# Performance work log

Measured on AMD Instinct MI355X. Metric: run time of the kernel, lower is better.

## Reference

```python
import jax, jax.numpy as jnp
import numpy as np

N = 50000   # num nodes
E = 800000  # num edges
D = 128     # in_features
C = 1.0     # curvature c
MIN_NORM = 1e-15
BALL_EPS = 4e-3  # float32 boundary eps in PoincareBall.proj


def setup_inputs() -> dict:
    key = jax.random.key(0)
    k1, k2 = jax.random.split(key)
    x = jax.random.normal(k1, (N, D), dtype=jnp.float32)
    edge_index = jax.random.randint(k2, (2, E), 0, N, dtype=jnp.int32)
    return {"x": x, "edge_index": edge_index}


def _expmap0(u, c):
    sqrt_c = c ** 0.5
    u_norm = jnp.maximum(jnp.linalg.norm(u, axis=-1, keepdims=True), MIN_NORM)
    return jnp.tanh(sqrt_c * u_norm) * u / (sqrt_c * u_norm)


def _proj(p, c):
    norm = jnp.maximum(jnp.linalg.norm(p, axis=-1, keepdims=True), MIN_NORM)
    maxnorm = (1.0 - BALL_EPS) / (c ** 0.5)
    return jnp.where(norm > maxnorm, p / norm * maxnorm, p)


def reference(x, edge_index):
    row, col = edge_index[0], edge_index[1]
    # add_remaining_self_loops: drop existing self-loops (weight->0), append N fresh self-loops w=1
    w = jnp.where(row == col, 0.0, 1.0).astype(x.dtype)
    loop = jnp.arange(N, dtype=row.dtype)
    row_f = jnp.concatenate([row, loop])
    col_f = jnp.concatenate([col, loop])
    w_f = jnp.concatenate([w, jnp.ones((N,), x.dtype)])
    # symmetric GCN normalization: D^{-1/2} A D^{-1/2}
    deg = jax.ops.segment_sum(w_f, row_f, num_segments=N)
    dis = jnp.where(deg > 0, 1.0 / jnp.sqrt(jnp.where(deg > 0, deg, 1.0)), 0.0)
    nw = dis[row_f] * w_f * dis[col_f]  # [E+N]
    # gather source features, weighted scatter-add into destination rows
    support = nw[:, None] * x[col_f]                       # [E+N, D]
    result = jax.ops.segment_sum(support, row_f, num_segments=N)  # [N, D]
    return _proj(_expmap0(result, C), C)
```

## Files before the change

### kernel.cpp

```cpp
#include <hip/hip_runtime.h>
#include <math.h>

#define N_NODES 50000
#define N_EDGES 800000
#define DFEAT   128
#define MAXNORM (1.0f - 4e-3f)
#define CAP     64
#define OVF_CAP 8192
#define NPART   8
#define PSIZE   (N_NODES / NPART)
#define SENT    N_NODES


__global__ void k_zero(int* __restrict__ deg, int* __restrict__ ovf_cnt, int n) {
    int i = blockIdx.x * blockDim.x + threadIdx.x;
    if (i < n) deg[i] = 0;
    if (i == 0) *ovf_cnt = 0;
}

__global__ void k_build(const int* __restrict__ row, const int* __restrict__ col,
                        int* __restrict__ deg, unsigned short* __restrict__ adj16,
                        int* __restrict__ ovf, int* __restrict__ ovf_cnt, int e) {
    int p      = blockIdx.x & (NPART - 1);
    int vblock = blockIdx.x >> 3;
    int stride = (gridDim.x >> 3) * blockDim.x;
    int lo = p * PSIZE, hi = lo + PSIZE;
    for (int i = vblock * blockDim.x + threadIdx.x; i < e; i += stride) {
        int r = row[i], c = col[i];
        if (r < lo || r >= hi || r == c) continue;
        int pos = atomicAdd(&deg[r], 1);
        if (pos < CAP) adj16[r * CAP + pos] = (unsigned short)c;
        else {
            int o = atomicAdd(ovf_cnt, 1);
            if (o < OVF_CAP) { ovf[2 * o] = r; ovf[2 * o + 1] = c; }
        }
    }
}

__global__ __launch_bounds__(256) void k_prep(const float* __restrict__ x,
                                              const int* __restrict__ deg,
                                              unsigned int* __restrict__ xb,
                                              int nthreads) {
    int t = blockIdx.x * blockDim.x + threadIdx.x;
    if (t >= nthreads) return;

    int node = t >> 4;
    int part = t & 15;
    unsigned int w[4];
    if (node < N_NODES) {
        float dis = rsqrtf((float)(deg[node] + 1));
        const float4* x4 = (const float4*)(x + (size_t)node * DFEAT + part * 8);
        float4 a = x4[0];
        float4 b = x4[1];
        float fs[8] = {a.x, a.y, a.z, a.w, b.x, b.y, b.z, b.w};
        #pragma unroll
        for (int k = 0; k < 4; ++k) {
            unsigned int lo = __float_as_uint(fs[2 * k] * dis);
            unsigned int hi = __float_as_uint(fs[2 * k + 1] * dis);
            lo = (lo + 0x7FFFu + ((lo >> 16) & 1u)) >> 16;
            hi = (hi + 0x7FFFu + ((hi >> 16) & 1u)) >> 16;
            w[k] = lo | (hi << 16);
        }
    } else {
        w[0] = w[1] = w[2] = w[3] = 0u;
    }
    ((uint4*)xb)[t] = make_uint4(w[0], w[1], w[2], w[3]);
}

__device__ __forceinline__ float bf_lo(unsigned int w) { return __uint_as_float(w << 16); }
__device__ __forceinline__ float bf_hi(unsigned int w) { return __uint_as_float(w & 0xFFFF0000u); }

__global__ __launch_bounds__(256) void k_gather_bf(const unsigned int* __restrict__ xb,
                                                   const unsigned short* __restrict__ adj16,
                                                   const int* __restrict__ deg,
                                                   const int* __restrict__ ovf,
                                                   const int* __restrict__ ovf_cnt,
                                                   float* __restrict__ out, int n) {
    int lane = threadIdx.x & 63;
    int half = lane >> 5;
    int fl   = lane & 31;
    int rowi = blockIdx.x * 4 + (threadIdx.x >> 6);
    if (rowi >= n) return;

    int cnt    = deg[rowi];
    int capcnt = cnt < CAP ? cnt : CAP;

    int a = SENT;
    if (lane < capcnt) a = (int)adj16[rowi * CAP + lane];

    const unsigned int* __restrict__ xw = xb + 2 * fl;

    float acc0 = 0.f, acc1 = 0.f, acc2 = 0.f, acc3 = 0.f;

    {
        int c[16];
        #pragma unroll
        for (int j = 0; j < 16; ++j) c[j] = __shfl(a, 2 * j + half);
        uint2 v[16];
        #pragma unroll
        for (int j = 0; j < 16; ++j) v[j] = *(const uint2*)(xw + c[j] * (DFEAT / 2));
        #pragma unroll
        for (int j = 0; j < 16; ++j) {
            acc0 += bf_lo(v[j].x); acc1 += bf_hi(v[j].x);
            acc2 += bf_lo(v[j].y); acc3 += bf_hi(v[j].y);
        }
    }
    if (capcnt > 32) {
        int c[16];
        #pragma unroll
        for (int j = 0; j < 16; ++j) c[j] = __shfl(a, 32 + 2 * j + half);
        uint2 v[16];
        #pragma unroll
        for (int j = 0; j < 16; ++j) v[j] = *(const uint2*)(xw + c[j] * (DFEAT / 2));
        #pragma unroll
        for (int j = 0; j < 16; ++j) {
            acc0 += bf_lo(v[j].x); acc1 += bf_hi(v[j].x);
            acc2 += bf_lo(v[j].y); acc3 += bf_hi(v[j].y);
        }
    }

    int novf = *ovf_cnt;
    if (novf > 0 && half == 0) {
        for (int k = 0; k < novf; ++k) {
            if (ovf[2 * k] == rowi) {
                uint2 v = *(const uint2*)(xw + ovf[2 * k + 1] * (DFEAT / 2));
                acc0 += bf_lo(v.x); acc1 += bf_hi(v.x);
                acc2 += bf_lo(v.y); acc3 += bf_hi(v.y);
            }
        }
    }

    acc0 += __shfl_xor(acc0, 32);
    acc1 += __shfl_xor(acc1, 32);
    acc2 += __shfl_xor(acc2, 32);
    acc3 += __shfl_xor(acc3, 32);

    uint2 sv = *(const uint2*)(xw + rowi * (DFEAT / 2));
    acc0 += bf_lo(sv.x); acc1 += bf_hi(sv.x);
    acc2 += bf_lo(sv.y); acc3 += bf_hi(sv.y);

    float di = rsqrtf((float)(cnt + 1));
    acc0 *= di; acc1 *= di; acc2 *= di; acc3 *= di;

    float nsq = acc0 * acc0 + acc1 * acc1 + acc2 * acc2 + acc3 * acc3;
    #pragma unroll
    for (int off = 16; off > 0; off >>= 1) nsq += __shfl_xor(nsq, off);

    float un = fmaxf(sqrtf(nsq), 1e-15f);
    float th = tanhf(un);
    float scale = th / un;
    if (th > MAXNORM) scale *= MAXNORM / th;

    if (half == 0) {
        float4 o = make_float4(acc0 * scale, acc1 * scale, acc2 * scale, acc3 * scale);
        *(float4*)(out + (size_t)rowi * DFEAT + 4 * fl) = o;
    }
}


#define SCAN_BLK 256
#define NUM_SCAN_BLOCKS ((N_NODES + SCAN_BLK - 1) / SCAN_BLK)

__global__ void k_init_deg(int* __restrict__ deg, int n) {
    int i = blockIdx.x * blockDim.x + threadIdx.x;
    if (i < n) deg[i] = 1;
}

__global__ void k_hist(const int* __restrict__ row, const int* __restrict__ col,
                       int* __restrict__ deg, int e) {
    int i = blockIdx.x * blockDim.x + threadIdx.x;
    if (i < e) {
        int r = row[i], c = col[i];
        if (r != c) atomicAdd(&deg[r], 1);
    }
}

__global__ __launch_bounds__(SCAN_BLK) void k_block_sums(const int* __restrict__ deg,
                                                         int* __restrict__ blockSums, int n) {
    __shared__ int s[SCAN_BLK];
    int t = threadIdx.x;
    int i = blockIdx.x * SCAN_BLK + t;
    s[t] = (i < n) ? (deg[i] - 1) : 0;
    __syncthreads();
    for (int off = SCAN_BLK / 2; off > 0; off >>= 1) {
        if (t < off) s[t] += s[t + off];
        __syncthreads();
    }
    if (t == 0) blockSums[blockIdx.x] = s[0];
}

__global__ __launch_bounds__(SCAN_BLK) void k_scan_blocks(const int* __restrict__ blockSums,
                                                          int* __restrict__ blockBase) {
    __shared__ int s[SCAN_BLK];
    int t = threadIdx.x;
    s[t] = (t < NUM_SCAN_BLOCKS) ? blockSums[t] : 0;
    __syncthreads();
    for (int off = 1; off < SCAN_BLK; off <<= 1) {
        int v = (t >= off) ? s[t - off] : 0;
        __syncthreads();
        s[t] += v;
        __syncthreads();
    }
    if (t < NUM_SCAN_BLOCKS) blockBase[t] = (t == 0) ? 0 : s[t - 1];
}

__global__ __launch_bounds__(SCAN_BLK) void k_block_scan(const int* __restrict__ deg,
                                                         const int* __restrict__ blockBase,
                                                         int* __restrict__ offs,
                                                         int* __restrict__ cursor, int n) {
    __shared__ int s[SCAN_BLK];
    int t = threadIdx.x;
    int i = blockIdx.x * SCAN_BLK + t;
    int cnt = (i < n) ? (deg[i] - 1) : 0;
    s[t] = cnt;
    __syncthreads();
    for (int off = 1; off < SCAN_BLK; off <<= 1) {
        int v = (t >= off) ? s[t - off] : 0;
        __syncthreads();
        s[t] += v;
        __syncthreads();
    }
    if (i < n) {
        int excl = s[t] - cnt + blockBase[blockIdx.x];
        offs[i]   = excl;
        cursor[i] = excl;
    }
}

__global__ void k_scatter(const int* __restrict__ row, const int* __restrict__ col,
                          int* __restrict__ cursor, int* __restrict__ adj, int e) {
    int i = blockIdx.x * blockDim.x + threadIdx.x;
    if (i < e) {
        int r = row[i], c = col[i];
        if (r != c) {
            int pos = atomicAdd(&cursor[r], 1);
            adj[pos] = c;
        }
    }
}

__global__ __launch_bounds__(256) void k_gather_csr(const float* __restrict__ x,
                                                    const int* __restrict__ adj,
                                                    const int* __restrict__ offs,
                                                    const int* __restrict__ deg,
                                                    float* __restrict__ out, int n) {
    int lane = threadIdx.x & 63;
    int rowi = blockIdx.x * 4 + (threadIdx.x >> 6);
    if (rowi >= n) return;

    const float2* __restrict__ x2 = (const float2*)x;
    int beg = offs[rowi];
    int cnt = deg[rowi] - 1;

    float2 acc = make_float2(0.0f, 0.0f);
    for (int base = 0; base < cnt; base += 64) {
        int m = cnt - base; if (m > 64) m = 64;
        int a = 0;
        if (lane < m) a = adj[beg + base + lane];
        for (int nb = 0; nb < m; ++nb) {
            int c = __shfl(a, nb);
            float w = rsqrtf((float)deg[c]);
            float2 v = x2[c * (DFEAT / 2) + lane];
            acc.x += w * v.x;
            acc.y += w * v.y;
        }
    }
    float di = rsqrtf((float)deg[rowi]);
    float2 self = x2[rowi * (DFEAT / 2) + lane];
    acc.x = di * (acc.x + di * self.x);
    acc.y = di * (acc.y + di * self.y);

    float nsq = acc.x * acc.x + acc.y * acc.y;
    #pragma unroll
    for (int off = 32; off > 0; off >>= 1) nsq += __shfl_xor(nsq, off);

    float un = fmaxf(sqrtf(nsq), 1e-15f);
    float th = tanhf(un);
    float scale = th / un;
    if (th > MAXNORM) scale *= MAXNORM / th;

    float2 o = make_float2(acc.x * scale, acc.y * scale);
    ((float2*)out)[rowi * (DFEAT / 2) + lane] = o;
}


extern "C" void kernel_launch(void* const* d_in, const int* in_sizes, int n_in,
                              void* d_out, int out_size, void* d_ws, size_t ws_size,
                              hipStream_t stream) {
    const float* x          = (const float*)d_in[0];
    const int*   edge_index = (const int*)d_in[1];
    const int*   row = edge_index;
    const int*   col = edge_index + N_EDGES;
    float* out = (float*)d_out;
    char*  ws  = (char*)d_ws;

    size_t sz_xb    = sizeof(unsigned short) * (size_t)(N_NODES + 1) * DFEAT;
    size_t sz_adj16 = sizeof(unsigned short) * (size_t)N_NODES * CAP;
    size_t sz_deg   = sizeof(int) * (size_t)N_NODES;
    size_t need = sz_xb + sz_adj16 + sz_deg + sizeof(int) * (1 + 2 * (size_t)OVF_CAP);

    dim3 blk(256);
    if (ws_size >= need) {
        size_t off = 0;
        unsigned int*   xb      = (unsigned int*)(ws + off);   off += sz_xb;
        unsigned short* adj16   = (unsigned short*)(ws + off); off += sz_adj16;
        int*            deg     = (int*)(ws + off);            off += sz_deg;
        int*            ovf_cnt = (int*)(ws + off);            off += sizeof(int);
        int*            ovf     = (int*)(ws + off);

        int nprep = (N_NODES + 1) * (DFEAT / 8);
        k_zero<<<dim3((N_NODES + 255) / 256), blk, 0, stream>>>(deg, ovf_cnt, N_NODES);
        k_build<<<dim3(8192), blk, 0, stream>>>(row, col, deg, adj16, ovf, ovf_cnt, N_EDGES);
        k_prep<<<dim3((nprep + 255) / 256), blk, 0, stream>>>(x, deg, xb, nprep);
        k_gather_bf<<<dim3((N_NODES + 3) / 4), blk, 0, stream>>>(xb, adj16, deg, ovf, ovf_cnt, out, N_NODES);
    } else {
        size_t off = 0;
        int* deg       = (int*)(ws + off); off += sizeof(int) * (size_t)N_NODES;
        int* offs      = (int*)(ws + off); off += sizeof(int) * (size_t)N_NODES;
        int* cursor    = (int*)(ws + off); off += sizeof(int) * (size_t)N_NODES;
        int* blockSums = (int*)(ws + off); off += sizeof(int) * (size_t)NUM_SCAN_BLOCKS;
        int* blockBase = (int*)(ws + off); off += sizeof(int) * (size_t)NUM_SCAN_BLOCKS;
        int* adj       = (int*)(ws + off);

        k_init_deg<<<dim3((N_NODES + 255) / 256), blk, 0, stream>>>(deg, N_NODES);
        k_hist<<<dim3((N_EDGES + 255) / 256), blk, 0, stream>>>(row, col, deg, N_EDGES);
        k_block_sums<<<dim3(NUM_SCAN_BLOCKS), dim3(SCAN_BLK), 0, stream>>>(deg, blockSums, N_NODES);
        k_scan_blocks<<<dim3(1), dim3(SCAN_BLK), 0, stream>>>(blockSums, blockBase);
        k_block_scan<<<dim3(NUM_SCAN_BLOCKS), dim3(SCAN_BLK), 0, stream>>>(deg, blockBase, offs, cursor, N_NODES);
        k_scatter<<<dim3((N_EDGES + 255) / 256), blk, 0, stream>>>(row, col, cursor, adj, N_EDGES);
        k_gather_csr<<<dim3((N_NODES + 3) / 4), blk, 0, stream>>>(x, adj, offs, deg, out, N_NODES);
    }
}
```

Before: 148.2 us.

## Shrink adjacency cap, vectorize edge reads, add nontemporal loads/stores, hoist self load

Halves the per-node adjacency capacity to 32, so the gather kernel issues two 8-wide load batches instead of two 16-wide batches. The build kernel now reads row and col as int4 and handles the remainder with a scalar tail. The x reads in prep and the output stores use nontemporal builtins, the self-feature load is hoisted ahead of the gather, and the overflow scan runs only for rows whose degree exceeds the cap. With a mean degree of about 16, more nodes will exceed 32 and spill to the overflow list, which each such row scans linearly. The overflow list is capped at 8192 entries, so if it fills, the extra edges are silently dropped.

```diff
diff --git a/kernel.cpp b/kernel.cpp
--- a/kernel.cpp
+++ b/kernel.cpp
@@ -5,17 +5,32 @@
 #define N_EDGES 800000
 #define DFEAT   128
 #define MAXNORM (1.0f - 4e-3f)
-#define CAP     64
+#define CAP     32
 #define OVF_CAP 8192
 #define NPART   8
 #define PSIZE   (N_NODES / NPART)
 #define SENT    N_NODES
 
+typedef float vfloat4 __attribute__((ext_vector_type(4)));
+
 
 __global__ void k_zero(int* __restrict__ deg, int* __restrict__ ovf_cnt, int n) {
     int i = blockIdx.x * blockDim.x + threadIdx.x;
     if (i < n) deg[i] = 0;
     if (i == 0) *ovf_cnt = 0;
+}
+
+__device__ __forceinline__ void build_edge(int r, int c, int lo, int hi,
+                                           int* __restrict__ deg,
+                                           unsigned short* __restrict__ adj16,
+                                           int* __restrict__ ovf, int* __restrict__ ovf_cnt) {
+    if (r < lo || r >= hi || r == c) return;
+    int pos = atomicAdd(&deg[r], 1);
+    if (pos < CAP) adj16[r * CAP + pos] = (unsigned short)c;
+    else {
+        int o = atomicAdd(ovf_cnt, 1);
+        if (o < OVF_CAP) { ovf[2 * o] = r; ovf[2 * o + 1] = c; }
+    }
 }
 
 __global__ void k_build(const int* __restrict__ row, const int* __restrict__ col,
@@ -23,18 +38,23 @@
                         int* __restrict__ ovf, int* __restrict__ ovf_cnt, int e) {
     int p      = blockIdx.x & (NPART - 1);
     int vblock = blockIdx.x >> 3;
-    int stride = (gridDim.x >> 3) * blockDim.x;
+    int tpp    = (gridDim.x >> 3) * blockDim.x;
+    int tid    = vblock * blockDim.x + threadIdx.x;
     int lo = p * PSIZE, hi = lo + PSIZE;
-    for (int i = vblock * blockDim.x + threadIdx.x; i < e; i += stride) {
-        int r = row[i], c = col[i];
-        if (r < lo || r >= hi || r == c) continue;
-        int pos = atomicAdd(&deg[r], 1);
-        if (pos < CAP) adj16[r * CAP + pos] = (unsigned short)c;
-        else {
-            int o = atomicAdd(ovf_cnt, 1);
-            if (o < OVF_CAP) { ovf[2 * o] = r; ovf[2 * o + 1] = c; }
-        }
-    }
+
+    int e4 = e >> 2;
+    const int4* __restrict__ row4 = (const int4*)row;
+    const int4* __restrict__ col4 = (const int4*)col;
+    for (int i = tid; i < e4; i += tpp) {
+        int4 r4 = row4[i];
+        int4 c4 = col4[i];
+        build_edge(r4.x, c4.x, lo, hi, deg, adj16, ovf, ovf_cnt);
+        build_edge(r4.y, c4.y, lo, hi, deg, adj16, ovf, ovf_cnt);
+        build_edge(r4.z, c4.z, lo, hi, deg, adj16, ovf, ovf_cnt);
+        build_edge(r4.w, c4.w, lo, hi, deg, adj16, ovf, ovf_cnt);
+    }
+    for (int i = (e4 << 2) + tid; i < e; i += tpp)
+        build_edge(row[i], col[i], lo, hi, deg, adj16, ovf, ovf_cnt);
 }
 
 __global__ __launch_bounds__(256) void k_prep(const float* __restrict__ x,
@@ -49,9 +69,9 @@
     unsigned int w[4];
     if (node < N_NODES) {
         float dis = rsqrtf((float)(deg[node] + 1));
-        const float4* x4 = (const float4*)(x + (size_t)node * DFEAT + part * 8);
-        float4 a = x4[0];
-        float4 b = x4[1];
+        const vfloat4* x4 = (const vfloat4*)(x + (size_t)node * DFEAT + part * 8);
+        vfloat4 a = __builtin_nontemporal_load(x4);
+        vfloat4 b = __builtin_nontemporal_load(x4 + 1);
         float fs[8] = {a.x, a.y, a.z, a.w, b.x, b.y, b.z, b.w};
         #pragma unroll
         for (int k = 0; k < 4; ++k) {
@@ -90,37 +110,39 @@
 
     const unsigned int* __restrict__ xw = xb + 2 * fl;
 
+    uint2 sv = *(const uint2*)(xw + rowi * (DFEAT / 2));
+
     float acc0 = 0.f, acc1 = 0.f, acc2 = 0.f, acc3 = 0.f;
 
     {
-        int c[16];
-        #pragma unroll
-        for (int j = 0; j < 16; ++j) c[j] = __shfl(a, 2 * j + half);
-        uint2 v[16];
-        #pragma unroll
-        for (int j = 0; j < 16; ++j) v[j] = *(const uint2*)(xw + c[j] * (DFEAT / 2));
-        #pragma unroll
-        for (int j = 0; j < 16; ++j) {
+        int c[8];
+        #pragma unroll
+        for (int j = 0; j < 8; ++j) c[j] = __shfl(a, 2 * j + half);
+        uint2 v[8];
+        #pragma unroll
+        for (int j = 0; j < 8; ++j) v[j] = *(const uint2*)(xw + c[j] * (DFEAT / 2));
+        #pragma unroll
+        for (int j = 0; j < 8; ++j) {
             acc0 += bf_lo(v[j].x); acc1 += bf_hi(v[j].x);
             acc2 += bf_lo(v[j].y); acc3 += bf_hi(v[j].y);
         }
     }
-    if (capcnt > 32) {
-        int c[16];
-        #pragma unroll
-        for (int j = 0; j < 16; ++j) c[j] = __shfl(a, 32 + 2 * j + half);
-        uint2 v[16];
-        #pragma unroll
-        for (int j = 0; j < 16; ++j) v[j] = *(const uint2*)(xw + c[j] * (DFEAT / 2));
-        #pragma unroll
-        for (int j = 0; j < 16; ++j) {
+    if (capcnt > 16) {
+        int c[8];
+        #pragma unroll
+        for (int j = 0; j < 8; ++j) c[j] = __shfl(a, 16 + 2 * j + half);
+        uint2 v[8];
+        #pragma unroll
+        for (int j = 0; j < 8; ++j) v[j] = *(const uint2*)(xw + c[j] * (DFEAT / 2));
+        #pragma unroll
+        for (int j = 0; j < 8; ++j) {
             acc0 += bf_lo(v[j].x); acc1 += bf_hi(v[j].x);
             acc2 += bf_lo(v[j].y); acc3 += bf_hi(v[j].y);
         }
     }
 
-    int novf = *ovf_cnt;
-    if (novf > 0 && half == 0) {
+    if (cnt > CAP && half == 0) {
+        int novf = *ovf_cnt;
         for (int k = 0; k < novf; ++k) {
             if (ovf[2 * k] == rowi) {
                 uint2 v = *(const uint2*)(xw + ovf[2 * k + 1] * (DFEAT / 2));
@@ -135,7 +157,6 @@
     acc2 += __shfl_xor(acc2, 32);
     acc3 += __shfl_xor(acc3, 32);
 
-    uint2 sv = *(const uint2*)(xw + rowi * (DFEAT / 2));
     acc0 += bf_lo(sv.x); acc1 += bf_hi(sv.x);
     acc2 += bf_lo(sv.y); acc3 += bf_hi(sv.y);
 
@@ -152,8 +173,8 @@
     if (th > MAXNORM) scale *= MAXNORM / th;
 
     if (half == 0) {
-        float4 o = make_float4(acc0 * scale, acc1 * scale, acc2 * scale, acc3 * scale);
-        *(float4*)(out + (size_t)rowi * DFEAT + 4 * fl) = o;
+        vfloat4 o = { acc0 * scale, acc1 * scale, acc2 * scale, acc3 * scale };
+        __builtin_nontemporal_store(o, (vfloat4*)(out + (size_t)rowi * DFEAT + 4 * fl));
     }
 }
 
```

Result: no change. 149.6 us (+1.0%).
